# Performance work log

Measured on AMD Instinct MI355X. Metric: run time of the kernel, lower is better.

## Reference

```python
import jax, jax.numpy as jnp
import numpy as np

B, CIN, COUT = 4, 512, 64
T, H, W = 16, 32, 32


def conv1x1(x, w, b=None):
    # 1x1x1 Conv3d == per-voxel linear: w (out, in), x (b, in, t, h, w)
    y = jnp.einsum('oc,bcthw->bothw', w, x)
    if b is not None:
        y = y + b[None, :, None, None, None]
    return y


def setup_inputs() -> dict:
    key = jax.random.key(0)
    ks = jax.random.split(key, 9)
    def kaiming(k, fan_out_shape):
        out_c, in_c = fan_out_shape
        std = np.sqrt(2.0 / out_c)  # fan_out mode for 1x1x1 kernel
        return jax.random.normal(k, fan_out_shape, dtype=jnp.float32) * std
    c4, c8 = CIN // 4, CIN // 8
    return {
        'x': jax.random.normal(ks[0], (B, CIN, T, H, W), dtype=jnp.float32),
        'w_add1': kaiming(ks[1], (CIN, CIN)), 'b_add1': jnp.zeros((CIN,), jnp.float32),
        'w_add2': kaiming(ks[2], (CIN, CIN)), 'b_add2': jnp.zeros((CIN,), jnp.float32),
        'w_occ1': kaiming(ks[3], (c4, CIN)), 'b_occ1': jnp.zeros((c4,), jnp.float32),
        'w_occ2': kaiming(ks[4], (c8, c4)), 'b_occ2': jnp.zeros((c8,), jnp.float32),
        'w_occ3': kaiming(ks[5], (COUT, c8)),  # bias=False
    }


def reference(x, w_add1, b_add1, w_add2, b_add2, w_occ1, b_occ1, w_occ2, b_occ2, w_occ3):
    # feature_map = add_on_layer(x): conv -> relu -> conv
    feat = conv1x1(jax.nn.relu(conv1x1(x, w_add1, b_add1)), w_add2, b_add2)
    # occ_map = abs(occ(x)): conv -> relu -> conv -> relu -> conv(no bias)
    h = jax.nn.relu(conv1x1(x, w_occ1, b_occ1))
    h = jax.nn.relu(conv1x1(h, w_occ2, b_occ2))
    occ = jnp.abs(conv1x1(h, w_occ3))  # (B, COUT, T, H, W)
    # output with pool='avg': mean over spatial of occ[:, :, None] * feat[:, None]
    # == einsum contraction over T*H*W, avoiding the (B,COUT,CIN,T,H,W) intermediate
    S = T * H * W
    out = jnp.einsum('bothw,bcthw->boc', occ, feat) / S  # (B, COUT, CIN)
    return out
```

## Files before the change

kernel.cpp:

```cpp
#include <hip/hip_runtime.h>


#define S_TOT 16384

typedef __attribute__((ext_vector_type(8))) short bf8_t;
typedef __attribute__((ext_vector_type(4))) short s4_t;
typedef __attribute__((ext_vector_type(4))) float f4_t;

#define MFMA __builtin_amdgcn_mfma_f32_16x16x32_bf16

__device__ __forceinline__ short f2bf(float f) {
  union { float f; unsigned u; } v; v.f = f;
  unsigned u = v.u + 0x7FFFu + ((v.u >> 16) & 1u);
  return (short)(u >> 16);
}

__device__ __forceinline__ void glds16(const void* g, void* l) {
  __builtin_amdgcn_global_load_lds(
      (const __attribute__((address_space(1))) void*)g,
      (__attribute__((address_space(3))) void*)l, 16, 0, 0);
}

__device__ __forceinline__ void stage16k(const short* g, short* lds,
                                         int wv, int lane) {
#pragma unroll
  for (int i = 0; i < 4; ++i) {
    const int off = (wv * 4 + i) * 512;
    glds16(g + off + lane * 8, lds + off);
  }
}

__global__ __launch_bounds__(256) void k_convert(
    const float* __restrict__ w1, const float* __restrict__ wo1,
    const float* __restrict__ wo2, const float* __restrict__ wo3,
    short* __restrict__ dst) {
  int i = blockIdx.x * 256 + threadIdx.x;
  if (i < 262144) {
    const int j = i >> 9, k = i & 511;
    const int di = ((j >> 7) * 8 + (k >> 6)) * 8192 + ((k >> 3) & 7) * 1024 +
                   (j & 127) * 8 + (k & 7);
    dst[di] = f2bf(w1[i]);
  } else if (i < 327680) {
    const int e = i - 262144;
    const int c4 = e >> 9, k = e & 511;
    const int di = 262144 + (k >> 6) * 8192 + ((k >> 3) & 7) * 1024 +
                   c4 * 8 + (k & 7);
    dst[di] = f2bf(wo1[e]);
  } else if (i < 335872) {
    dst[i] = f2bf(wo2[i - 327680]);
  } else if (i < 339968) {
    dst[i] = f2bf(wo3[i - 335872]);
  }
}

__global__ __launch_bounds__(256) void k_transpose(
    const float* __restrict__ x, short* __restrict__ xTs) {
  __shared__ float tls[64][65];
  const int sb = blockIdx.x, cb = blockIdx.y, b = blockIdx.z;
  const int t = threadIdx.x;
  {
    const int cr = t >> 2, ss = (t & 3) * 16;
    const float* src = x + ((size_t)b * 512 + cb * 64 + cr) * S_TOT + sb * 64 + ss;
    f4_t v0 = *(const f4_t*)(src);
    f4_t v1 = *(const f4_t*)(src + 4);
    f4_t v2 = *(const f4_t*)(src + 8);
    f4_t v3 = *(const f4_t*)(src + 12);
#pragma unroll
    for (int j = 0; j < 4; ++j) {
      tls[cr][ss + j]      = v0[j];
      tls[cr][ss + 4 + j]  = v1[j];
      tls[cr][ss + 8 + j]  = v2[j];
      tls[cr][ss + 12 + j] = v3[j];
    }
  }
  __syncthreads();
  {
    const int sr = t >> 2, cs = (t & 3) * 16;
    alignas(16) short tmp[16];
#pragma unroll
    for (int j = 0; j < 16; ++j) tmp[j] = f2bf(tls[cs + j][sr]);
    const int st = sb >> 1, s_in = (sb & 1) * 64 + sr, k8 = cs >> 3;
    short* base = xTs + (((size_t)(b * 128 + st) * 8 + cb) * 8 + k8) * 1024 +
                  s_in * 8;
    *(bf8_t*)base          = *(const bf8_t*)&tmp[0];
    *(bf8_t*)(base + 1024) = *(const bf8_t*)&tmp[8];
  }
}

__global__ __launch_bounds__(256) void k_occ(
    const short* __restrict__ xTs, const short* __restrict__ wo1,
    const short* __restrict__ wo2, const short* __restrict__ wo3,
    const float* __restrict__ bo1, const float* __restrict__ bo2,
    short* __restrict__ occP, float* __restrict__ sumocc) {
  __shared__ short smem[32768];
  short* const buf0 = smem;
  short* const buf1 = smem + 16384;
  short* const h1s = buf0;
  short* const h2s = buf1;
  const int tile = blockIdx.x, b = blockIdx.y;
  const int t = threadIdx.x, lane = t & 63, wv = t >> 6;
  const int q = lane >> 4, li = lane & 15;
  const int mh = (wv & 1) * 64, nh = (wv >> 1) * 64;
  const short* xTb = xTs + (size_t)(b * 128 + tile) * 65536;
  const f4_t fz = {0.f, 0.f, 0.f, 0.f};

  f4_t acc[4][4];
#pragma unroll
  for (int i = 0; i < 4; ++i)
#pragma unroll
    for (int j = 0; j < 4; ++j) acc[i][j] = fz;

  stage16k(xTb, buf1, wv, lane);
  stage16k(wo1, buf1 + 8192, wv, lane);
  int cur = 1;
  for (int i = 0; i < 8; ++i) {
    __syncthreads();
    if (i < 7) {
      short* nb_ = cur ? buf0 : buf1;
      stage16k(xTb + (i + 1) * 8192, nb_, wv, lane);
      stage16k(wo1 + (i + 1) * 8192, nb_ + 8192, wv, lane);
    }
    const short* xs = cur ? buf1 : buf0;
    const short* wsp = xs + 8192;
#pragma unroll
    for (int kk = 0; kk < 2; ++kk) {
      const int pl = (4 * kk + q) * 128;
      bf8_t a[4], bb[4];
#pragma unroll
      for (int ma = 0; ma < 4; ++ma)
        a[ma] = *(const bf8_t*)&wsp[(pl + mh + 16 * ma + li) * 8];
#pragma unroll
      for (int nb = 0; nb < 4; ++nb)
        bb[nb] = *(const bf8_t*)&xs[(pl + nh + 16 * nb + li) * 8];
#pragma unroll
      for (int ma = 0; ma < 4; ++ma)
#pragma unroll
        for (int nb = 0; nb < 4; ++nb)
          acc[ma][nb] = MFMA(a[ma], bb[nb], acc[ma][nb], 0, 0, 0);
    }
    cur ^= 1;
  }
  __syncthreads();
#pragma unroll
  for (int ma = 0; ma < 4; ++ma) {
    const int c40 = mh + 16 * ma + 4 * q;
    f4_t bv = *(const f4_t*)(bo1 + c40);
#pragma unroll
    for (int nb = 0; nb < 4; ++nb) {
      const int sl = nh + 16 * nb + li;
      s4_t p;
#pragma unroll
      for (int r = 0; r < 4; ++r) p[r] = f2bf(fmaxf(acc[ma][nb][r] + bv[r], 0.0f));
      *(s4_t*)&h1s[((c40 >> 3) * 128 + sl) * 8 + (c40 & 7)] = p;
    }
  }
  __syncthreads();
  f4_t a2[4][2];
#pragma unroll
  for (int i = 0; i < 4; ++i) { a2[i][0] = fz; a2[i][1] = fz; }
#pragma unroll
  for (int kk = 0; kk < 4; ++kk) {
    const int pl = (4 * kk + q) * 128;
    bf8_t a[4], bb[2];
#pragma unroll
    for (int ma = 0; ma < 4; ++ma)
      a[ma] = *(const bf8_t*)(wo2 + (size_t)(16 * ma + li) * 128 + kk * 32 + q * 8);
#pragma unroll
    for (int nb = 0; nb < 2; ++nb)
      bb[nb] = *(const bf8_t*)&h1s[(pl + 32 * wv + 16 * nb + li) * 8];
#pragma unroll
    for (int ma = 0; ma < 4; ++ma)
#pragma unroll
      for (int nb = 0; nb < 2; ++nb)
        a2[ma][nb] = MFMA(a[ma], bb[nb], a2[ma][nb], 0, 0, 0);
  }
#pragma unroll
  for (int ma = 0; ma < 4; ++ma) {
    const int c80 = 16 * ma + 4 * q;
    f4_t bv = *(const f4_t*)(bo2 + c80);
#pragma unroll
    for (int nb = 0; nb < 2; ++nb) {
      const int sl = 32 * wv + 16 * nb + li;
      s4_t p;
#pragma unroll
      for (int r = 0; r < 4; ++r) p[r] = f2bf(fmaxf(a2[ma][nb][r] + bv[r], 0.0f));
      *(s4_t*)&h2s[((c80 >> 3) * 128 + sl) * 8 + (c80 & 7)] = p;
    }
  }
  f4_t a3[4][2];
#pragma unroll
  for (int i = 0; i < 4; ++i) { a3[i][0] = fz; a3[i][1] = fz; }
#pragma unroll
  for (int kk = 0; kk < 2; ++kk) {
    const int pl = (4 * kk + q) * 128;
    bf8_t a[4], bb[2];
#pragma unroll
    for (int ma = 0; ma < 4; ++ma)
      a[ma] = *(const bf8_t*)(wo3 + (size_t)(16 * ma + li) * 64 + kk * 32 + q * 8);
#pragma unroll
    for (int nb = 0; nb < 2; ++nb)
      bb[nb] = *(const bf8_t*)&h2s[(pl + 32 * wv + 16 * nb + li) * 8];
#pragma unroll
    for (int ma = 0; ma < 4; ++ma)
#pragma unroll
      for (int nb = 0; nb < 2; ++nb)
        a3[ma][nb] = MFMA(a[ma], bb[nb], a3[ma][nb], 0, 0, 0);
  }
  short* ot = occP + (size_t)(b * 128 + tile) * 8192;
#pragma unroll
  for (int ma = 0; ma < 4; ++ma)
#pragma unroll
    for (int nb = 0; nb < 2; ++nb) {
      const int o = 16 * ma + 4 * q;
      const int sl = 32 * wv + 16 * nb + li;
#pragma unroll
      for (int r = 0; r < 4; ++r)
        ot[(sl >> 3) * 512 + (o + r) * 8 + (sl & 7)] = f2bf(fabsf(a3[ma][nb][r]));
    }
#pragma unroll
  for (int ma = 0; ma < 4; ++ma)
#pragma unroll
    for (int r = 0; r < 4; ++r) {
      float v = fabsf(a3[ma][0][r]) + fabsf(a3[ma][1][r]);
#pragma unroll
      for (int m = 1; m < 16; m <<= 1) v += __shfl_xor(v, m, 64);
      if (li == 0) atomicAdd(&sumocc[b * 64 + 16 * ma + 4 * q + r], v);
    }
}

__global__ __launch_bounds__(256) void k_feat(
    const short* __restrict__ xTs, const short* __restrict__ w1s,
    const float* __restrict__ b1, const short* __restrict__ occP,
    float* __restrict__ M) {
  __shared__ short smem[32768];
  short* const buf0 = smem;
  short* const buf1 = smem + 16384;
  short* const r1s = buf0;
  const int sg = blockIdx.x, cb = blockIdx.y, b = blockIdx.z;
  const int t = threadIdx.x, lane = t & 63, wv = t >> 6;
  const int q = lane >> 4, li = lane & 15;
  const int mh = (wv & 1) * 64, nh = (wv >> 1) * 64;
  const short* w1b = w1s + (size_t)cb * 65536;
  const f4_t fz = {0.f, 0.f, 0.f, 0.f};

  float biasv[4];
#pragma unroll
  for (int nb = 0; nb < 4; ++nb) biasv[nb] = b1[cb * 128 + nh + 16 * nb + li];

  f4_t macc[4][2];
#pragma unroll
  for (int i = 0; i < 4; ++i) { macc[i][0] = fz; macc[i][1] = fz; }

  {
    const short* xT0 = xTs + (size_t)(b * 128 + sg * 4) * 65536;
    stage16k(xT0, buf1, wv, lane);
    stage16k(w1b, buf1 + 8192, wv, lane);
  }

  for (int tt = 0; tt < 4; ++tt) {
    const int st = sg * 4 + tt;
    const short* xTb = xTs + (size_t)(b * 128 + st) * 65536;
    f4_t acc[4][4];
#pragma unroll
    for (int i = 0; i < 4; ++i)
#pragma unroll
      for (int j = 0; j < 4; ++j) acc[i][j] = fz;

    int cur = 1;
    for (int i = 0; i < 8; ++i) {
      __syncthreads();
      if (i < 7) {
        short* nb_ = cur ? buf0 : buf1;
        stage16k(xTb + (i + 1) * 8192, nb_, wv, lane);
        stage16k(w1b + (i + 1) * 8192, nb_ + 8192, wv, lane);
      }
      const short* xs = cur ? buf1 : buf0;
      const short* wsp = xs + 8192;
#pragma unroll
      for (int kk = 0; kk < 2; ++kk) {
        const int pl = (4 * kk + q) * 128;
        bf8_t a[4], bb[4];
#pragma unroll
        for (int ma = 0; ma < 4; ++ma)
          a[ma] = *(const bf8_t*)&xs[(pl + mh + 16 * ma + li) * 8];
#pragma unroll
        for (int nb = 0; nb < 4; ++nb)
          bb[nb] = *(const bf8_t*)&wsp[(pl + nh + 16 * nb + li) * 8];
#pragma unroll
        for (int ma = 0; ma < 4; ++ma)
#pragma unroll
          for (int nb = 0; nb < 4; ++nb)
            acc[ma][nb] = MFMA(a[ma], bb[nb], acc[ma][nb], 0, 0, 0);
      }
      cur ^= 1;
    }
    __syncthreads();
#pragma unroll
    for (int ma = 0; ma < 4; ++ma) {
      const int sl0 = mh + 16 * ma + 4 * q;
#pragma unroll
      for (int nb = 0; nb < 4; ++nb) {
        const int jl = nh + 16 * nb + li;
        s4_t p;
#pragma unroll
        for (int r = 0; r < 4; ++r)
          p[r] = f2bf(fmaxf(acc[ma][nb][r] + biasv[nb], 0.0f));
        *(s4_t*)&r1s[((sl0 >> 3) * 128 + jl) * 8 + (sl0 & 7)] = p;
      }
    }
    __syncthreads();
    if (tt < 3) {
      stage16k(xTb + 65536, buf1, wv, lane);
      stage16k(w1b, buf1 + 8192, wv, lane);
    }
    const short* ot = occP + (size_t)(b * 128 + st) * 8192;
    bf8_t af[4][4];
#pragma unroll
    for (int kc = 0; kc < 4; ++kc)
#pragma unroll
      for (int ma = 0; ma < 4; ++ma)
        af[ma][kc] = *(const bf8_t*)(ot + ((kc * 4 + q) * 64 + 16 * ma + li) * 8);
#pragma unroll
    for (int kc = 0; kc < 4; ++kc) {
      const int pl = (4 * kc + q) * 128;
      bf8_t bb[2];
#pragma unroll
      for (int nb = 0; nb < 2; ++nb)
        bb[nb] = *(const bf8_t*)&r1s[(pl + 32 * wv + 16 * nb + li) * 8];
#pragma unroll
      for (int ma = 0; ma < 4; ++ma)
#pragma unroll
        for (int nb = 0; nb < 2; ++nb)
          macc[ma][nb] = MFMA(af[ma][kc], bb[nb], macc[ma][nb], 0, 0, 0);
    }
  }
#pragma unroll
  for (int ma = 0; ma < 4; ++ma)
#pragma unroll
    for (int nb = 0; nb < 2; ++nb) {
      const int jg = cb * 128 + 32 * wv + 16 * nb + li;
#pragma unroll
      for (int r = 0; r < 4; ++r) {
        const int o = 16 * ma + 4 * q + r;
        atomicAdd(&M[((size_t)b * 64 + o) * 512 + jg], macc[ma][nb][r]);
      }
    }
}

__global__ __launch_bounds__(256) void k_out(
    const float* __restrict__ M, const float* __restrict__ sumocc,
    const float* __restrict__ w2, const float* __restrict__ b2,
    float* __restrict__ out) {
  const int cg = blockIdx.x, og = blockIdx.y, b = blockIdx.z;
  const int t = threadIdx.x;
  const int o = og * 16 + (t >> 4);
  const int c = cg * 16 + (t & 15);
  const float* mr = M + ((size_t)b * 64 + o) * 512;
  const float* wr = w2 + (size_t)c * 512;
  float a = 0.0f;
  for (int j = 0; j < 512; j += 4) {
    f4_t mv = *(const f4_t*)(mr + j);
    f4_t wv = *(const f4_t*)(wr + j);
    a += mv[0] * wv[0] + mv[1] * wv[1] + mv[2] * wv[2] + mv[3] * wv[3];
  }
  out[((size_t)b * 64 + o) * 512 + c] =
      (a + sumocc[b * 64 + o] * b2[c]) * (1.0f / 16384.0f);
}

extern "C" void kernel_launch(void* const* d_in, const int* in_sizes, int n_in,
                              void* d_out, int out_size, void* d_ws, size_t ws_size,
                              hipStream_t stream) {
  (void)in_sizes; (void)n_in; (void)out_size; (void)ws_size;
  const float* x      = (const float*)d_in[0];
  const float* w_add1 = (const float*)d_in[1];
  const float* b_add1 = (const float*)d_in[2];
  const float* w_add2 = (const float*)d_in[3];
  const float* b_add2 = (const float*)d_in[4];
  const float* w_occ1 = (const float*)d_in[5];
  const float* b_occ1 = (const float*)d_in[6];
  const float* w_occ2 = (const float*)d_in[7];
  const float* b_occ2 = (const float*)d_in[8];
  const float* w_occ3 = (const float*)d_in[9];

  char* ws = (char*)d_ws;
  short* xTs     = (short*)(ws);
  short* wb      = (short*)(ws + 67108864);
  short* occP    = (short*)(ws + 67788800);
  float* M       = (float*)(ws + 76177408);
  float* sumocc  = (float*)(ws + 76701696);

  hipMemsetAsync(M, 0, 524288 + 1024, stream);
  k_convert<<<dim3(1328), dim3(256), 0, stream>>>(w_add1, w_occ1, w_occ2, w_occ3, wb);
  k_transpose<<<dim3(256, 8, 4), dim3(256), 0, stream>>>(x, xTs);

  const short* w1sp = wb;
  const short* wbo1 = wb + 262144;
  const short* wbo2 = wb + 327680;
  const short* wbo3 = wb + 335872;
  k_occ<<<dim3(128, 4), dim3(256), 0, stream>>>(xTs, wbo1, wbo2, wbo3,
                                                b_occ1, b_occ2, occP, sumocc);
  k_feat<<<dim3(32, 4, 4), dim3(256), 0, stream>>>(xTs, w1sp, b_add1, occP, M);
  k_out<<<dim3(32, 4, 4), dim3(256), 0, stream>>>(M, sumocc, w_add2, b_add2,
                                                  (float*)d_out);
}
```

Baseline: 403.4 us.

## Load MFMA fragments directly from global memory instead of LDS staging

The two big GEMM loops in k_occ and k_feat no longer stage x and weight tiles into LDS through global_load_lds. Each wave now reads its bf16 fragments straight from global memory, double-buffered in registers, and the per-step barriers go away. LDS use drops and launch_bounds asks for 2 blocks per CU to raise occupancy. The cost is that data shared across waves is reloaded by each wave through L1/L2 rather than reused from LDS, and the register pressure may be higher.

```diff
diff --git a/kernel.cpp b/kernel.cpp
--- a/kernel.cpp
+++ b/kernel.cpp
@@ -15,19 +15,16 @@
   return (short)(u >> 16);
 }
 
-__device__ __forceinline__ void glds16(const void* g, void* l) {
-  __builtin_amdgcn_global_load_lds(
-      (const __attribute__((address_space(1))) void*)g,
-      (__attribute__((address_space(3))) void*)l, 16, 0, 0);
-}
-
-__device__ __forceinline__ void stage16k(const short* g, short* lds,
-                                         int wv, int lane) {
-#pragma unroll
-  for (int i = 0; i < 4; ++i) {
-    const int off = (wv * 4 + i) * 512;
-    glds16(g + off + lane * 8, lds + off);
-  }
+__device__ __forceinline__ void load_frags(const short* __restrict__ arow,
+                                           const short* __restrict__ brow,
+                                           int s, int q, bf8_t* A, bf8_t* B) {
+  const int off = (s >> 1) * 8192 + ((s & 1) * 4 + q) * 1024;
+#pragma unroll
+  for (int ma = 0; ma < 4; ++ma)
+    A[ma] = *(const bf8_t*)(arow + off + ma * 128);
+#pragma unroll
+  for (int nb = 0; nb < 4; ++nb)
+    B[nb] = *(const bf8_t*)(brow + off + nb * 128);
 }
 
 __global__ __launch_bounds__(256) void k_convert(
@@ -87,16 +84,14 @@
   }
 }
 
-__global__ __launch_bounds__(256) void k_occ(
+__global__ __launch_bounds__(256, 2) void k_occ(
     const short* __restrict__ xTs, const short* __restrict__ wo1,
     const short* __restrict__ wo2, const short* __restrict__ wo3,
     const float* __restrict__ bo1, const float* __restrict__ bo2,
     short* __restrict__ occP, float* __restrict__ sumocc) {
-  __shared__ short smem[32768];
-  short* const buf0 = smem;
-  short* const buf1 = smem + 16384;
-  short* const h1s = buf0;
-  short* const h2s = buf1;
+  __shared__ short smem[24576];
+  short* const h1s = smem;
+  short* const h2s = smem + 16384;
   const int tile = blockIdx.x, b = blockIdx.y;
   const int t = threadIdx.x, lane = t & 63, wv = t >> 6;
   const int q = lane >> 4, li = lane & 15;
@@ -109,38 +104,24 @@
   for (int i = 0; i < 4; ++i)
 #pragma unroll
     for (int j = 0; j < 4; ++j) acc[i][j] = fz;
-
-  stage16k(xTb, buf1, wv, lane);
-  stage16k(wo1, buf1 + 8192, wv, lane);
-  int cur = 1;
-  for (int i = 0; i < 8; ++i) {
-    __syncthreads();
-    if (i < 7) {
-      short* nb_ = cur ? buf0 : buf1;
-      stage16k(xTb + (i + 1) * 8192, nb_, wv, lane);
-      stage16k(wo1 + (i + 1) * 8192, nb_ + 8192, wv, lane);
-    }
-    const short* xs = cur ? buf1 : buf0;
-    const short* wsp = xs + 8192;
-#pragma unroll
-    for (int kk = 0; kk < 2; ++kk) {
-      const int pl = (4 * kk + q) * 128;
-      bf8_t a[4], bb[4];
+  {
+    const short* arow = wo1 + (mh + li) * 8;
+    const short* brow = xTb + (nh + li) * 8;
+    bf8_t a0[4], b0[4], a1[4], b1[4];
+    load_frags(arow, brow, 0, q, a0, b0);
+#pragma unroll
+    for (int s = 0; s < 16; ++s) {
+      bf8_t* ca = (s & 1) ? a1 : a0;
+      bf8_t* cb = (s & 1) ? b1 : b0;
+      if (s < 15)
+        load_frags(arow, brow, s + 1, q, (s & 1) ? a0 : a1, (s & 1) ? b0 : b1);
 #pragma unroll
       for (int ma = 0; ma < 4; ++ma)
-        a[ma] = *(const bf8_t*)&wsp[(pl + mh + 16 * ma + li) * 8];
-#pragma unroll
-      for (int nb = 0; nb < 4; ++nb)
-        bb[nb] = *(const bf8_t*)&xs[(pl + nh + 16 * nb + li) * 8];
-#pragma unroll
-      for (int ma = 0; ma < 4; ++ma)
 #pragma unroll
         for (int nb = 0; nb < 4; ++nb)
-          acc[ma][nb] = MFMA(a[ma], bb[nb], acc[ma][nb], 0, 0, 0);
-    }
-    cur ^= 1;
-  }
-  __syncthreads();
+          acc[ma][nb] = MFMA(ca[ma], cb[nb], acc[ma][nb], 0, 0, 0);
+    }
+  }
 #pragma unroll
   for (int ma = 0; ma < 4; ++ma) {
     const int c40 = mh + 16 * ma + 4 * q;
@@ -228,14 +209,11 @@
     }
 }
 
-__global__ __launch_bounds__(256) void k_feat(
+__global__ __launch_bounds__(256, 2) void k_feat(
     const short* __restrict__ xTs, const short* __restrict__ w1s,
     const float* __restrict__ b1, const short* __restrict__ occP,
     float* __restrict__ M) {
-  __shared__ short smem[32768];
-  short* const buf0 = smem;
-  short* const buf1 = smem + 16384;
-  short* const r1s = buf0;
+  __shared__ short r1s[16384];
   const int sg = blockIdx.x, cb = blockIdx.y, b = blockIdx.z;
   const int t = threadIdx.x, lane = t & 63, wv = t >> 6;
   const int q = lane >> 4, li = lane & 15;
@@ -251,11 +229,7 @@
 #pragma unroll
   for (int i = 0; i < 4; ++i) { macc[i][0] = fz; macc[i][1] = fz; }
 
-  {
-    const short* xT0 = xTs + (size_t)(b * 128 + sg * 4) * 65536;
-    stage16k(xT0, buf1, wv, lane);
-    stage16k(w1b, buf1 + 8192, wv, lane);
-  }
+  const short* browW = w1b + (nh + li) * 8;
 
   for (int tt = 0; tt < 4; ++tt) {
     const int st = sg * 4 + tt;
@@ -266,33 +240,23 @@
 #pragma unroll
       for (int j = 0; j < 4; ++j) acc[i][j] = fz;
 
-    int cur = 1;
-    for (int i = 0; i < 8; ++i) {
-      __syncthreads();
-      if (i < 7) {
-        short* nb_ = cur ? buf0 : buf1;
-        stage16k(xTb + (i + 1) * 8192, nb_, wv, lane);
-        stage16k(w1b + (i + 1) * 8192, nb_ + 8192, wv, lane);
+    {
+      const short* arow = xTb + (mh + li) * 8;
+      bf8_t a0[4], b0[4], a1[4], b1f[4];
+      load_frags(arow, browW, 0, q, a0, b0);
+#pragma unroll
+      for (int s = 0; s < 16; ++s) {
+        bf8_t* ca = (s & 1) ? a1 : a0;
+        bf8_t* cbf = (s & 1) ? b1f : b0;
+        if (s < 15)
+          load_frags(arow, browW, s + 1, q, (s & 1) ? a0 : a1,
+                     (s & 1) ? b0 : b1f);
+#pragma unroll
+        for (int ma = 0; ma < 4; ++ma)
+#pragma unroll
+          for (int nb = 0; nb < 4; ++nb)
+            acc[ma][nb] = MFMA(ca[ma], cbf[nb], acc[ma][nb], 0, 0, 0);
       }
-      const short* xs = cur ? buf1 : buf0;
-      const short* wsp = xs + 8192;
-#pragma unroll
-      for (int kk = 0; kk < 2; ++kk) {
-        const int pl = (4 * kk + q) * 128;
-        bf8_t a[4], bb[4];
-#pragma unroll
-        for (int ma = 0; ma < 4; ++ma)
-          a[ma] = *(const bf8_t*)&xs[(pl + mh + 16 * ma + li) * 8];
-#pragma unroll
-        for (int nb = 0; nb < 4; ++nb)
-          bb[nb] = *(const bf8_t*)&wsp[(pl + nh + 16 * nb + li) * 8];
-#pragma unroll
-        for (int ma = 0; ma < 4; ++ma)
-#pragma unroll
-          for (int nb = 0; nb < 4; ++nb)
-            acc[ma][nb] = MFMA(a[ma], bb[nb], acc[ma][nb], 0, 0, 0);
-      }
-      cur ^= 1;
     }
     __syncthreads();
 #pragma unroll
@@ -309,29 +273,21 @@
       }
     }
     __syncthreads();
-    if (tt < 3) {
-      stage16k(xTb + 65536, buf1, wv, lane);
-      stage16k(w1b, buf1 + 8192, wv, lane);
-    }
     const short* ot = occP + (size_t)(b * 128 + st) * 8192;
-    bf8_t af[4][4];
-#pragma unroll
-    for (int kc = 0; kc < 4; ++kc)
+#pragma unroll
+    for (int kc = 0; kc < 4; ++kc) {
+      bf8_t af[4], bb[2];
 #pragma unroll
       for (int ma = 0; ma < 4; ++ma)
-        af[ma][kc] = *(const bf8_t*)(ot + ((kc * 4 + q) * 64 + 16 * ma + li) * 8);
-#pragma unroll
-    for (int kc = 0; kc < 4; ++kc) {
-      const int pl = (4 * kc + q) * 128;
-      bf8_t bb[2];
+        af[ma] = *(const bf8_t*)(ot + ((kc * 4 + q) * 64 + 16 * ma + li) * 8);
 #pragma unroll
       for (int nb = 0; nb < 2; ++nb)
-        bb[nb] = *(const bf8_t*)&r1s[(pl + 32 * wv + 16 * nb + li) * 8];
+        bb[nb] = *(const bf8_t*)&r1s[((4 * kc + q) * 128 + 32 * wv + 16 * nb + li) * 8];
 #pragma unroll
       for (int ma = 0; ma < 4; ++ma)
 #pragma unroll
         for (int nb = 0; nb < 2; ++nb)
-          macc[ma][nb] = MFMA(af[ma][kc], bb[nb], macc[ma][nb], 0, 0, 0);
+          macc[ma][nb] = MFMA(af[ma], bb[nb], macc[ma][nb], 0, 0, 0);
     }
   }
 #pragma unroll
```

New measurement: 476.6 us. +18.1%, slower.
